# Kernel optimization log

Measured on AMD Instinct MI355X. Metric: run time of the kernel, lower is better.

## Reference

```python
import jax, jax.numpy as jnp
import numpy as np
import math

B = 512
EMB = 512
CLASSNUM = 70722
M = 0.4
H = 0.333
S = 64.0
EPS = 1e-3


def setup_inputs() -> dict:
    key = jax.random.key(0)
    k1, k2, k3, k4, k5 = jax.random.split(key, 5)
    embbedings = jax.random.normal(k1, (B, EMB), dtype=jnp.float32)
    # feature norms: positive, realistic range ~[1, 30)
    norms = jax.random.uniform(k2, (B, 1), dtype=jnp.float32) * 29.0 + 1.0
    label = jax.random.randint(k3, (B,), 0, CLASSNUM, dtype=jnp.int64)
    class_sample_num_ = jax.random.uniform(k4, (B,), dtype=jnp.float32) * 9.0 + 1.0
    kernel = jax.random.normal(k5, (EMB, CLASSNUM), dtype=jnp.float32)
    return {
        "embbedings": embbedings,
        "norms": norms,
        "label": label,
        "class_sample_num_": class_sample_num_,
        "kernel": kernel,
    }


def reference(embbedings, norms, label, class_sample_num_, kernel):
    # l2-normalize kernel columns (axis=0)
    kernel_norm = kernel / jnp.linalg.norm(kernel, axis=0, keepdims=True)
    cosine = jnp.matmul(embbedings, kernel_norm)  # [B, C]
    cosine = jnp.clip(cosine, -1.0 + EPS, 1.0 - EPS)

    # detached margin scaler path (torch uses .detach / no_grad)
    safe_norms = jnp.clip(norms, 0.001, 100.0)
    safe_norms = safe_norms / (class_sample_num_[:, None] + 0.001)
    safe_norms = jnp.clip(safe_norms, 0.001, 100.0)
    safe_norms = jax.lax.stop_gradient(safe_norms)

    mean = jnp.mean(safe_norms)
    std = jnp.std(safe_norms, ddof=1)  # torch.std is unbiased
    # t_alpha = 1.0 => batch stats are exactly this batch's mean/std
    batch_mean, batch_std = mean, std

    margin_scaler = (safe_norms - batch_mean) / (batch_std + EPS)
    margin_scaler = jnp.clip(margin_scaler * H, -1.0, 1.0)  # [B, 1]
    ms = margin_scaler[:, 0]  # [B]

    rows = jnp.arange(B)
    lab = label.astype(jnp.int32)

    # angular margin: theta_m = clip(theta + onehot * (-m*ms))
    theta = jnp.arccos(cosine)
    theta = theta.at[rows, lab].add(-M * ms)
    theta_m = jnp.clip(theta, EPS, math.pi - EPS)
    cosine2 = jnp.cos(theta_m)

    # additive margin at the label column: g_add = m + m*ms
    cosine2 = cosine2.at[rows, lab].add(-(M + M * ms))

    return cosine2 * S
```

## Files before the change

kernel.cpp:

```cpp
#include <hip/hip_runtime.h>
#include <math.h>

#define CLASSNUM 70722
#define BATCH 512
#define EMBD 512
#define M_C 0.4f
#define H_C 0.333f
#define S_C 64.0f
#define EPS_C 0.001f
#define PI_F 3.14159265358979f

typedef __bf16 bf16_t;
typedef __bf16 bf16x4 __attribute__((ext_vector_type(4)));
typedef __bf16 bf16x8 __attribute__((ext_vector_type(8)));
typedef float f32x4 __attribute__((ext_vector_type(4)));

__device__ __forceinline__ float clampf(float x, float lo, float hi) {
    return fminf(fmaxf(x, lo), hi);
}

__global__ __launch_bounds__(256) void prep_kernel(
    const float* __restrict__ emb, const float* __restrict__ norms,
    const float* __restrict__ csn, bf16_t* __restrict__ Aws,
    float* __restrict__ msw)
{
    __shared__ float sred[256];
    const int tid = threadIdx.x;
    if (blockIdx.x == 0) {
        float s0, s1;
        {
            float sn = clampf(norms[tid], 0.001f, 100.0f);
            sn = sn / (csn[tid] + 0.001f);
            s0 = clampf(sn, 0.001f, 100.0f);
        }
        {
            float sn = clampf(norms[tid + 256], 0.001f, 100.0f);
            sn = sn / (csn[tid + 256] + 0.001f);
            s1 = clampf(sn, 0.001f, 100.0f);
        }
        sred[tid] = s0 + s1;
        __syncthreads();
        for (int off = 128; off > 0; off >>= 1) {
            if (tid < off) sred[tid] += sred[tid + off];
            __syncthreads();
        }
        const float mean = sred[0] * (1.0f / 512.0f);
        __syncthreads();
        const float d0 = s0 - mean, d1 = s1 - mean;
        sred[tid] = d0 * d0 + d1 * d1;
        __syncthreads();
        for (int off = 128; off > 0; off >>= 1) {
            if (tid < off) sred[tid] += sred[tid + off];
            __syncthreads();
        }
        const float stdv = sqrtf(sred[0] * (1.0f / 511.0f));
        const float inv = 1.0f / (stdv + EPS_C);
        msw[tid]       = clampf(d0 * inv * H_C, -1.0f, 1.0f);
        msw[tid + 256] = clampf(d1 * inv * H_C, -1.0f, 1.0f);
    } else {
        const int G = (blockIdx.x - 1) * 256 + tid;
        const int kt = G >> 11;
        const int rem = G & 2047;
        const int rg = rem >> 6;
        const int lane = rem & 63;
        const int row = rg * 16 + (lane & 15);
        const int k0 = kt * 32 + (lane >> 4) * 8;
        const float* src = emb + row * EMBD + k0;
        const float4 v0 = *(const float4*)src;
        const float4 v1 = *(const float4*)(src + 4);
        bf16x8 bw;
        bw[0] = (bf16_t)v0.x; bw[1] = (bf16_t)v0.y;
        bw[2] = (bf16_t)v0.z; bw[3] = (bf16_t)v0.w;
        bw[4] = (bf16_t)v1.x; bw[5] = (bf16_t)v1.y;
        bw[6] = (bf16_t)v1.z; bw[7] = (bf16_t)v1.w;
        *(bf16x8*)(Aws + (size_t)G * 8) = bw;
    }
}


#define LOADB4(t, dst) do {                                             \
    const size_t ko_ = (size_t)((t) * 32) * CLASSNUM;                   \
    _Pragma("unroll")                                                   \
    for (int j_ = 0; j_ < 4; ++j_)                                      \
        dst[j_] = bp[ko_ + (size_t)j_ * CLASSNUM];                      \
} while (0)

#define LOADA4(t, af) do {                                              \
    const bf16x8* ap_ = (const bf16x8*)Aws                              \
        + (((t) * 32 + wave * 4) * 64 + lane);                          \
    _Pragma("unroll")                                                   \
    for (int mi_ = 0; mi_ < 4; ++mi_) af[mi_] = ap_[mi_ * 64];          \
} while (0)

#define CVTW(src, buf) do {                                             \
    bf16x4 w_;                                                          \
    _Pragma("unroll")                                                   \
    for (int j_ = 0; j_ < 4; ++j_) {                                    \
        const float v_ = src[j_];                                       \
        ssq = fmaf(v_, v_, ssq);                                        \
        w_[j_] = (bf16_t)v_;                                            \
    }                                                                   \
    *(bf16x4*)&Blds[buf][c * 40 + kg * 4] = w_;                         \
} while (0)

#define MFMA16(af, buf) do {                                            \
    bf16x8 bfr_[4];                                                     \
    _Pragma("unroll")                                                   \
    for (int ni_ = 0; ni_ < 4; ++ni_)                                   \
        bfr_[ni_] = *(const bf16x8*)                                    \
            &Blds[buf][(ni_ * 16 + r16) * 40 + quad * 8];               \
    __builtin_amdgcn_s_setprio(1);                                      \
    _Pragma("unroll")                                                   \
    for (int mi_ = 0; mi_ < 4; ++mi_)                                   \
        _Pragma("unroll")                                               \
        for (int ni_ = 0; ni_ < 4; ++ni_)                               \
            acc[mi_][ni_] = __builtin_amdgcn_mfma_f32_16x16x32_bf16(    \
                af[mi_], bfr_[ni_], acc[mi_][ni_], 0, 0, 0);            \
    __builtin_amdgcn_s_setprio(0);                                      \
} while (0)

#define BARRIER() do {                                                  \
    asm volatile("s_waitcnt lgkmcnt(0)" ::: "memory");                  \
    __builtin_amdgcn_s_barrier();                                       \
} while (0)

__global__ __launch_bounds__(512, 4) void gemm_kernel(
    const bf16_t* __restrict__ Aws, const float* __restrict__ Kmat,
    const float* __restrict__ emb, const int* __restrict__ label,
    const float* __restrict__ msw, float* __restrict__ out)
{
    __shared__ bf16_t Blds[2][64 * 40];
    __shared__ float red[512];
    __shared__ float invn_s[64];
    __shared__ int   lab_s[BATCH];
    __shared__ float lo_s[BATCH];

    const int tid  = threadIdx.x;
    const int lane = tid & 63;
    const int wave = tid >> 6;
    const int r16  = lane & 15;
    const int quad = lane >> 4;

    const int nwg = (CLASSNUM + 63) / 64;
    const int q_ = nwg >> 3, r_ = nwg & 7;
    const int xcd = blockIdx.x & 7, idx = blockIdx.x >> 3;
    const int nb = (xcd < r_) ? (xcd * (q_ + 1) + idx)
                              : (r_ * (q_ + 1) + (xcd - r_) * q_ + idx);
    const int n0 = nb * 64;

    lab_s[tid] = label[tid];

    const int c  = tid & 63;
    const int kg = tid >> 6;
    int cg = n0 + c;
    if (cg >= CLASSNUM) cg = CLASSNUM - 1;
    const float* bp = Kmat + (size_t)(kg * 4) * CLASSNUM + cg;

    f32x4 acc[4][4];
    const f32x4 zero = {0.0f, 0.0f, 0.0f, 0.0f};
#pragma unroll
    for (int i = 0; i < 4; ++i)
#pragma unroll
        for (int j = 0; j < 4; ++j) acc[i][j] = zero;
    float ssq = 0.0f;

    float bv0[4], bv1[4];
    bf16x8 af[4];

    LOADA4(0, af);
    LOADB4(0, bv0);
    LOADB4(1, bv1);
    CVTW(bv0, 0);
    BARRIER();

#pragma unroll 1
    for (int p = 0; p < 8; ++p) {
        {
            MFMA16(af, 0);
            LOADA4(2 * p + 1, af);
            if (p < 7) LOADB4(2 * p + 2, bv0);
            CVTW(bv1, 1);
            BARRIER();
        }
        {
            MFMA16(af, 1);
            if (p < 7) {
                LOADA4(2 * p + 2, af);
                LOADB4(2 * p + 3, bv1);
                CVTW(bv0, 0);
            }
            BARRIER();
        }
    }

    red[tid] = ssq;
    __syncthreads();
    if (tid < 64) {
        float s = 0.0f;
#pragma unroll
        for (int g = 0; g < 8; ++g) s += red[tid + g * 64];
        invn_s[tid] = (s > 0.0f) ? (1.0f / sqrtf(s)) : 0.0f;
    }

#pragma unroll 1
    for (int b = wave; b < BATCH; b += 8) {
        const int lc = lab_s[b];
        if (lc >= n0 && lc < n0 + 64) {
            const float* col = Kmat + lc;
            const float* e = emb + b * EMBD;
            float dot = 0.0f, ss = 0.0f;
#pragma unroll
            for (int k = lane; k < EMBD; k += 64) {
                const float kv = col[(size_t)k * CLASSNUM];
                dot = fmaf(e[k], kv, dot);
                ss  = fmaf(kv, kv, ss);
            }
            for (int off = 32; off > 0; off >>= 1) {
                dot += __shfl_down(dot, off);
                ss  += __shfl_down(ss, off);
            }
            if (lane == 0) {
                float cc = dot / sqrtf(ss);
                cc = clampf(cc, -1.0f + EPS_C, 1.0f - EPS_C);
                const float msv = msw[b];
                float th = acosf(cc) - M_C * msv;
                th = clampf(th, EPS_C, PI_F - EPS_C);
                lo_s[b] = (cosf(th) - (M_C + M_C * msv)) * S_C;
            }
        }
    }
    __syncthreads();

#pragma unroll
    for (int mi = 0; mi < 4; ++mi) {
#pragma unroll
        for (int rr = 0; rr < 4; ++rr) {
            const int row = wave * 64 + mi * 16 + quad * 4 + rr;
            const int labc = lab_s[row];
            const float lov = lo_s[row];
            float* orow = out + (size_t)row * CLASSNUM;
#pragma unroll
            for (int ni = 0; ni < 4; ++ni) {
                const int col_loc = ni * 16 + r16;
                const int col = n0 + col_loc;
                if (col < CLASSNUM) {
                    const float cc = clampf(acc[mi][ni][rr] * invn_s[col_loc],
                                            -1.0f + EPS_C, 1.0f - EPS_C);
                    float v = cc * S_C;
                    if (labc == col) v = lov;
                    orow[col] = v;
                }
            }
        }
    }
}

extern "C" void kernel_launch(void* const* d_in, const int* in_sizes, int n_in,
                              void* d_out, int out_size, void* d_ws, size_t ws_size,
                              hipStream_t stream)
{
    const float* emb   = (const float*)d_in[0];
    const float* norms = (const float*)d_in[1];
    const int*   label = (const int*)d_in[2];
    const float* csn   = (const float*)d_in[3];
    const float* kmat  = (const float*)d_in[4];
    float* out = (float*)d_out;

    const size_t A_BYTES = (size_t)BATCH * EMBD * sizeof(bf16_t);
    if (ws_size < A_BYTES + 4096) return;
    bf16_t* Aws = (bf16_t*)d_ws;
    float* msw  = (float*)((char*)d_ws + A_BYTES);

    prep_kernel<<<129, 256, 0, stream>>>(emb, norms, csn, Aws, msw);
    const int nblk = (CLASSNUM + 63) / 64;
    gemm_kernel<<<nblk, 512, 0, stream>>>(Aws, kmat, emb, label, msw, out);
}
```

Before: 325.0 us.

## Deepen GEMM K-stage to 64 and move label-column margin to separate kernel

The GEMM main loop now stages 64 K-values per LDS buffer instead of 32, halving the number of barriers and issuing wider 8-element loads and stores per thread. The per-block label-column recomputation, a serial loop over all 512 rows, is moved into a dedicated lab_kernel that runs before the GEMM and feeds the result through the workspace. The s_setprio hints are removed. A scatter kernel is added even though the GEMM epilogue already writes the label values, which adds an extra launch. LDS use grows, which may lower occupancy.

Result: slower. 468.1 us (+44.0%).

```diff
diff --git a/kernel.cpp b/kernel.cpp
--- a/kernel.cpp
+++ b/kernel.cpp
@@ -11,7 +11,6 @@
 #define PI_F 3.14159265358979f
 
 typedef __bf16 bf16_t;
-typedef __bf16 bf16x4 __attribute__((ext_vector_type(4)));
 typedef __bf16 bf16x8 __attribute__((ext_vector_type(8)));
 typedef float f32x4 __attribute__((ext_vector_type(4)));
 
@@ -77,46 +76,86 @@
     }
 }
 
-
-#define LOADB4(t, dst) do {                                             \
-    const size_t ko_ = (size_t)((t) * 32) * CLASSNUM;                   \
-    _Pragma("unroll")                                                   \
-    for (int j_ = 0; j_ < 4; ++j_)                                      \
+__global__ __launch_bounds__(256) void lab_kernel(
+    const float* __restrict__ emb, const int* __restrict__ label,
+    const float* __restrict__ kmat, const float* __restrict__ msw,
+    float* __restrict__ labout)
+{
+    __shared__ float red[256];
+    const int b = blockIdx.x;
+    const int tid = threadIdx.x;
+    const int lab = label[b];
+    const float* col = kmat + lab;
+    const float* e = emb + b * EMBD;
+    float dot = 0.0f, ss = 0.0f;
+#pragma unroll
+    for (int k = tid; k < EMBD; k += 256) {
+        const float kv = col[(size_t)k * CLASSNUM];
+        dot = fmaf(e[k], kv, dot);
+        ss  = fmaf(kv, kv, ss);
+    }
+    red[tid] = dot;
+    __syncthreads();
+    for (int off = 128; off > 0; off >>= 1) {
+        if (tid < off) red[tid] += red[tid + off];
+        __syncthreads();
+    }
+    const float dotT = red[0];
+    __syncthreads();
+    red[tid] = ss;
+    __syncthreads();
+    for (int off = 128; off > 0; off >>= 1) {
+        if (tid < off) red[tid] += red[tid + off];
+        __syncthreads();
+    }
+    if (tid == 0) {
+        float c = dotT / sqrtf(red[0]);
+        c = clampf(c, -1.0f + EPS_C, 1.0f - EPS_C);
+        const float msv = msw[b];
+        float th = acosf(c) - M_C * msv;
+        th = clampf(th, EPS_C, PI_F - EPS_C);
+        labout[b] = (cosf(th) - (M_C + M_C * msv)) * S_C;
+    }
+}
+
+
+#define LOADB8(t, dst) do {                                             \
+    const size_t ko_ = (size_t)((t) * 64) * CLASSNUM;                   \
+    _Pragma("unroll")                                                   \
+    for (int j_ = 0; j_ < 8; ++j_)                                      \
         dst[j_] = bp[ko_ + (size_t)j_ * CLASSNUM];                      \
 } while (0)
 
-#define LOADA4(t, af) do {                                              \
+#define LOADA4(t2, af) do {                                             \
     const bf16x8* ap_ = (const bf16x8*)Aws                              \
-        + (((t) * 32 + wave * 4) * 64 + lane);                          \
+        + (((t2) * 32 + wave * 4) * 64 + lane);                         \
     _Pragma("unroll")                                                   \
     for (int mi_ = 0; mi_ < 4; ++mi_) af[mi_] = ap_[mi_ * 64];          \
 } while (0)
 
-#define CVTW(src, buf) do {                                             \
-    bf16x4 w_;                                                          \
-    _Pragma("unroll")                                                   \
-    for (int j_ = 0; j_ < 4; ++j_) {                                    \
+#define CVTW8(src, buf) do {                                            \
+    bf16x8 w_;                                                          \
+    _Pragma("unroll")                                                   \
+    for (int j_ = 0; j_ < 8; ++j_) {                                    \
         const float v_ = src[j_];                                       \
         ssq = fmaf(v_, v_, ssq);                                        \
         w_[j_] = (bf16_t)v_;                                            \
     }                                                                   \
-    *(bf16x4*)&Blds[buf][c * 40 + kg * 4] = w_;                         \
-} while (0)
-
-#define MFMA16(af, buf) do {                                            \
+    *(bf16x8*)&Blds[buf][c * 72 + kg * 8] = w_;                         \
+} while (0)
+
+#define MFMA16K(af, buf, kk) do {                                       \
     bf16x8 bfr_[4];                                                     \
     _Pragma("unroll")                                                   \
     for (int ni_ = 0; ni_ < 4; ++ni_)                                   \
         bfr_[ni_] = *(const bf16x8*)                                    \
-            &Blds[buf][(ni_ * 16 + r16) * 40 + quad * 8];               \
-    __builtin_amdgcn_s_setprio(1);                                      \
+            &Blds[buf][(ni_ * 16 + r16) * 72 + (kk) * 32 + quad * 8];   \
     _Pragma("unroll")                                                   \
     for (int mi_ = 0; mi_ < 4; ++mi_)                                   \
         _Pragma("unroll")                                               \
         for (int ni_ = 0; ni_ < 4; ++ni_)                               \
             acc[mi_][ni_] = __builtin_amdgcn_mfma_f32_16x16x32_bf16(    \
                 af[mi_], bfr_[ni_], acc[mi_][ni_], 0, 0, 0);            \
-    __builtin_amdgcn_s_setprio(0);                                      \
 } while (0)
 
 #define BARRIER() do {                                                  \
@@ -126,10 +165,10 @@
 
 __global__ __launch_bounds__(512, 4) void gemm_kernel(
     const bf16_t* __restrict__ Aws, const float* __restrict__ Kmat,
-    const float* __restrict__ emb, const int* __restrict__ label,
-    const float* __restrict__ msw, float* __restrict__ out)
-{
-    __shared__ bf16_t Blds[2][64 * 40];
+    const int* __restrict__ label, const float* __restrict__ labout,
+    float* __restrict__ out)
+{
+    __shared__ bf16_t Blds[2][64 * 72];
     __shared__ float red[512];
     __shared__ float invn_s[64];
     __shared__ int   lab_s[BATCH];
@@ -149,12 +188,13 @@
     const int n0 = nb * 64;
 
     lab_s[tid] = label[tid];
+    lo_s[tid]  = labout[tid];
 
     const int c  = tid & 63;
     const int kg = tid >> 6;
     int cg = n0 + c;
     if (cg >= CLASSNUM) cg = CLASSNUM - 1;
-    const float* bp = Kmat + (size_t)(kg * 4) * CLASSNUM + cg;
+    const float* bp = Kmat + (size_t)(kg * 8) * CLASSNUM + cg;
 
     f32x4 acc[4][4];
     const f32x4 zero = {0.0f, 0.0f, 0.0f, 0.0f};
@@ -164,30 +204,34 @@
         for (int j = 0; j < 4; ++j) acc[i][j] = zero;
     float ssq = 0.0f;
 
-    float bv0[4], bv1[4];
+    float bv0[8], bv1[8];
     bf16x8 af[4];
 
     LOADA4(0, af);
-    LOADB4(0, bv0);
-    LOADB4(1, bv1);
-    CVTW(bv0, 0);
+    LOADB8(0, bv0);
+    LOADB8(1, bv1);
+    CVTW8(bv0, 0);
     BARRIER();
 
 #pragma unroll 1
-    for (int p = 0; p < 8; ++p) {
+    for (int p = 0; p < 4; ++p) {
         {
-            MFMA16(af, 0);
-            LOADA4(2 * p + 1, af);
-            if (p < 7) LOADB4(2 * p + 2, bv0);
-            CVTW(bv1, 1);
+            MFMA16K(af, 0, 0);
+            LOADA4(4 * p + 1, af);
+            MFMA16K(af, 0, 1);
+            CVTW8(bv1, 1);
+            LOADA4(4 * p + 2, af);
+            if (p < 3) LOADB8(2 * p + 2, bv0);
             BARRIER();
         }
         {
-            MFMA16(af, 1);
-            if (p < 7) {
-                LOADA4(2 * p + 2, af);
-                LOADB4(2 * p + 3, bv1);
-                CVTW(bv0, 0);
+            MFMA16K(af, 1, 0);
+            LOADA4(4 * p + 3, af);
+            MFMA16K(af, 1, 1);
+            if (p < 3) {
+                CVTW8(bv0, 0);
+                LOADA4(4 * p + 4, af);
+                LOADB8(2 * p + 3, bv1);
             }
             BARRIER();
         }
@@ -200,34 +244,6 @@
 #pragma unroll
         for (int g = 0; g < 8; ++g) s += red[tid + g * 64];
         invn_s[tid] = (s > 0.0f) ? (1.0f / sqrtf(s)) : 0.0f;
-    }
-
-#pragma unroll 1
-    for (int b = wave; b < BATCH; b += 8) {
-        const int lc = lab_s[b];
-        if (lc >= n0 && lc < n0 + 64) {
-            const float* col = Kmat + lc;
-            const float* e = emb + b * EMBD;
-            float dot = 0.0f, ss = 0.0f;
-#pragma unroll
-            for (int k = lane; k < EMBD; k += 64) {
-                const float kv = col[(size_t)k * CLASSNUM];
-                dot = fmaf(e[k], kv, dot);
-                ss  = fmaf(kv, kv, ss);
-            }
-            for (int off = 32; off > 0; off >>= 1) {
-                dot += __shfl_down(dot, off);
-                ss  += __shfl_down(ss, off);
-            }
-            if (lane == 0) {
-                float cc = dot / sqrtf(ss);
-                cc = clampf(cc, -1.0f + EPS_C, 1.0f - EPS_C);
-                const float msv = msw[b];
-                float th = acosf(cc) - M_C * msv;
-                th = clampf(th, EPS_C, PI_F - EPS_C);
-                lo_s[b] = (cosf(th) - (M_C + M_C * msv)) * S_C;
-            }
-        }
     }
     __syncthreads();
 
@@ -255,6 +271,14 @@
     }
 }
 
+__global__ __launch_bounds__(512) void scatter_kernel(
+    const int* __restrict__ label, const float* __restrict__ labout,
+    float* __restrict__ out)
+{
+    const int t = threadIdx.x;
+    out[(size_t)t * CLASSNUM + label[t]] = labout[t];
+}
+
 extern "C" void kernel_launch(void* const* d_in, const int* in_sizes, int n_in,
                               void* d_out, int out_size, void* d_ws, size_t ws_size,
                               hipStream_t stream)
@@ -268,10 +292,13 @@
 
     const size_t A_BYTES = (size_t)BATCH * EMBD * sizeof(bf16_t);
     if (ws_size < A_BYTES + 4096) return;
-    bf16_t* Aws = (bf16_t*)d_ws;
-    float* msw  = (float*)((char*)d_ws + A_BYTES);
+    bf16_t* Aws   = (bf16_t*)d_ws;
+    float* msw    = (float*)((char*)d_ws + A_BYTES);
+    float* labout = (float*)((char*)d_ws + A_BYTES + 2048);
 
     prep_kernel<<<129, 256, 0, stream>>>(emb, norms, csn, Aws, msw);
+    lab_kernel<<<BATCH, 256, 0, stream>>>(emb, label, kmat, msw, labout);
     const int nblk = (CLASSNUM + 63) / 64;
-    gemm_kernel<<<nblk, 512, 0, stream>>>(Aws, kmat, emb, label, msw, out);
-}
+    gemm_kernel<<<nblk, 512, 0, stream>>>(Aws, kmat, label, labout, out);
+    scatter_kernel<<<1, 512, 0, stream>>>(label, labout, out);
+}
```
